# Optimization experiments

Hardware: AMD Instinct MI355X
Metric: run time of the kernel (lower is better)

Reference implementation:

```python
import jax, jax.numpy as jnp
import numpy as np
import math

B, T, E, H = 64, 256, 1024, 16
HD = E // H  # 64
EPS = 1e-5


def layernorm(x, g, b):
    mu = jnp.mean(x, axis=-1, keepdims=True)
    var = jnp.mean(jnp.square(x - mu), axis=-1, keepdims=True)
    return (x - mu) * jax.lax.rsqrt(var + EPS) * g + b


def setup_inputs() -> dict:
    key = jax.random.key(0)
    ks = jax.random.split(key, 10)
    s = 0.02
    return {
        "x": jax.random.normal(ks[0], (B, T, E), dtype=jnp.float32),
        "ln1_g": jnp.ones((E,), jnp.float32),
        "ln1_b": jnp.zeros((E,), jnp.float32),
        "wk": jax.random.normal(ks[1], (H, E, HD), jnp.float32) * s,
        "wq": jax.random.normal(ks[2], (H, E, HD), jnp.float32) * s,
        "wv": jax.random.normal(ks[3], (H, E, HD), jnp.float32) * s,
        "w_proj": jax.random.normal(ks[4], (E, E), jnp.float32) * s,
        "b_proj": jnp.zeros((E,), jnp.float32),
        "ln2_g": jnp.ones((E,), jnp.float32),
        "ln2_b": jnp.zeros((E,), jnp.float32),
        "w1": jax.random.normal(ks[5], (E, E), jnp.float32) * s,
        "b1": jnp.zeros((E,), jnp.float32),
        "w2": jax.random.normal(ks[6], (E, E), jnp.float32) * s,
        "b2": jnp.zeros((E,), jnp.float32),
    }


def reference(x, ln1_g, ln1_b, wk, wq, wv, w_proj, b_proj, ln2_g, ln2_b, w1, b1, w2, b2):
    # --- multi-head causal attention on LN1(x) ---
    h = layernorm(x, ln1_g, ln1_b)
    k = jnp.einsum('bte,hed->bhtd', h, wk)
    q = jnp.einsum('bte,hed->bhtd', h, wq)
    v = jnp.einsum('bte,hed->bhtd', h, wv)
    # NOTE: original computes k @ q^T (K.Q^T), not the standard Q.K^T -- kept faithful
    scores = jnp.einsum('bhtd,bhsd->bhts', k, q) / math.sqrt(HD)
    mask = jnp.tril(jnp.ones((T, T), dtype=bool))
    scores = jnp.where(mask, scores, -jnp.inf)
    attn_w = jax.nn.softmax(scores, axis=-1)  # dropout = identity in eval
    attn = jnp.einsum('bhts,bhsd->bhtd', attn_w, v)
    attn = attn.transpose(0, 2, 1, 3).reshape(B, T, E)  # concat heads
    x = x + attn @ w_proj + b_proj
    # --- feed-forward on LN2(x) ---
    h2 = layernorm(x, ln2_g, ln2_b)
    ff = jax.nn.relu(h2 @ w1 + b1) @ w2 + b2
    return x + ff
```

## Files before the change

kernel.cpp:

```cpp
#include <hip/hip_runtime.h>

typedef unsigned int u32;
typedef unsigned short u16;
typedef __attribute__((ext_vector_type(8))) short bf16x8;
typedef __attribute__((ext_vector_type(4))) short bf16x4;
typedef __attribute__((ext_vector_type(4))) float f32x4;

#if defined(__has_builtin)
#if __has_builtin(__builtin_amdgcn_mfma_f32_16x16x16bf16_1k)
#define HAVE_MFMA16_1K 1
#endif
#endif

#define GLOBAL_AS __attribute__((address_space(1)))
#define LDS_AS    __attribute__((address_space(3)))

#define B_   64
#define T_   256
#define E_   1024
#define H_   16
#define HD_  64
#define NTOK (B_*T_)
#define K_   1024
#define LNEPS 1e-5f

__device__ __forceinline__ u16 f2bf(float f){
  u32 x = __float_as_uint(f);
  u32 r = x + 0x7fffu + ((x >> 16) & 1u);
  return (u16)(r >> 16);
}
__device__ __forceinline__ u16 f2bf_trunc(float f){
  return (u16)(__float_as_uint(f) >> 16);
}
__device__ __forceinline__ u32 pack2(float a, float b){
  return (u32)f2bf(a) | ((u32)f2bf(b) << 16);
}

__device__ __forceinline__ void gload16(const u16* g, u16* l){
  __builtin_amdgcn_global_load_lds((const GLOBAL_AS void*)g, (LDS_AS void*)l, 16, 0, 0);
}

__global__ __launch_bounds__(256) void ln_bf16_kernel(
    const float* __restrict__ x, const float* __restrict__ g,
    const float* __restrict__ b, u16* __restrict__ o)
{
  int lane  = threadIdx.x & 63;
  int token = (blockIdx.x << 2) + (threadIdx.x >> 6);
  const float4* xr = (const float4*)(x + (size_t)token * E_);
  float4 v[4];
  float s = 0.f, ss = 0.f;
  #pragma unroll
  for (int i = 0; i < 4; ++i){
    v[i] = xr[lane + 64 * i];
    s += v[i].x + v[i].y + v[i].z + v[i].w;
    ss = fmaf(v[i].x, v[i].x, fmaf(v[i].y, v[i].y,
         fmaf(v[i].z, v[i].z, fmaf(v[i].w, v[i].w, ss))));
  }
  #pragma unroll
  for (int off = 32; off > 0; off >>= 1){
    s  += __shfl_xor(s,  off);
    ss += __shfl_xor(ss, off);
  }
  float mu   = s * (1.f / E_);
  float var  = ss * (1.f / E_) - mu * mu;
  float rstd = rsqrtf(var + LNEPS);
  const float4* gr = (const float4*)g;
  const float4* br = (const float4*)b;
  uint2* orow = (uint2*)(o + (size_t)token * E_);
  #pragma unroll
  for (int i = 0; i < 4; ++i){
    float4 gg = gr[lane + 64 * i], bb = br[lane + 64 * i];
    float y0 = (v[i].x - mu) * rstd * gg.x + bb.x;
    float y1 = (v[i].y - mu) * rstd * gg.y + bb.y;
    float y2 = (v[i].z - mu) * rstd * gg.z + bb.z;
    float y3 = (v[i].w - mu) * rstd * gg.w + bb.w;
    orow[lane + 64 * i] = make_uint2(pack2(y0, y1), pack2(y2, y3));
  }
}

__global__ __launch_bounds__(256) void convq_kernel(
    const float* __restrict__ wk, const float* __restrict__ wq,
    const float* __restrict__ wv, u16* __restrict__ o)
{
  __shared__ float tile[64 * 68];
  const int zh = blockIdx.x, z = zh >> 4, h = zh & 15;
  const int k0 = blockIdx.y << 6;
  const float* w = (z == 0 ? wk : z == 1 ? wq : wv) + (size_t)h * (E_ * HD_);
  const float qs = (z == 1) ? 0.125f : 1.0f;
  const int t = threadIdx.x;
  {
    int kr = t >> 2, d0 = (t & 3) << 4;
    const float4* src = (const float4*)(w + (size_t)(k0 + kr) * HD_ + d0);
    #pragma unroll
    for (int i = 0; i < 4; ++i)
      *(float4*)(tile + kr * 68 + d0 + 4 * i) = src[i];
  }
  __syncthreads();
  {
    const size_t nb32 = (size_t)zh * 32 + (k0 >> 5);
    #pragma unroll
    for (int u = 0; u < 2; ++u) {
      int cid = t * 2 + u;
      int dd = cid >> 3, kc = cid & 7;
      u32 wd[4];
      #pragma unroll
      for (int e2 = 0; e2 < 4; ++e2)
        wd[e2] = pack2(qs * tile[(kc * 8 + 2 * e2) * 68 + dd],
                       qs * tile[(kc * 8 + 2 * e2 + 1) * 68 + dd]);
      u16* dst = o + (nb32 + (kc >> 2)) * 2048 + (size_t)(dd >> 4) * 512
                   + (size_t)(((kc & 3) << 4) + (dd & 15)) * 8;
      *(uint4*)dst = make_uint4(wd[0], wd[1], wd[2], wd[3]);
    }
  }
}

__global__ __launch_bounds__(256) void convt3_kernel(
    const float* __restrict__ wp, const float* __restrict__ w1,
    const float* __restrict__ w2, u16* __restrict__ op,
    u16* __restrict__ o1, u16* __restrict__ o2)
{
  __shared__ float tile[64 * 68];
  const int z = blockIdx.z;
  const float* w = (z == 0 ? wp : z == 1 ? w1 : w2);
  u16* o = (z == 0 ? op : z == 1 ? o1 : o2);
  const int n0 = blockIdx.x << 6, k0 = blockIdx.y << 6;
  const int t = threadIdx.x;
  {
    int kr = t >> 2, nn = (t & 3) << 4;
    const float4* src = (const float4*)(w + (size_t)(k0 + kr) * E_ + n0 + nn);
    #pragma unroll
    for (int i = 0; i < 4; ++i)
      *(float4*)(tile + kr * 68 + nn + 4 * i) = src[i];
  }
  __syncthreads();
  {
    const size_t nb32 = (size_t)(n0 >> 6) * 32 + (k0 >> 5);
    #pragma unroll
    for (int u = 0; u < 2; ++u) {
      int cid = t * 2 + u;
      int dd = cid >> 3, kc = cid & 7;
      u32 wd[4];
      #pragma unroll
      for (int e2 = 0; e2 < 4; ++e2)
        wd[e2] = pack2(tile[(kc * 8 + 2 * e2) * 68 + dd],
                       tile[(kc * 8 + 2 * e2 + 1) * 68 + dd]);
      u16* dst = o + (nb32 + (kc >> 2)) * 2048 + (size_t)(dd >> 4) * 512
                   + (size_t)(((kc & 3) << 4) + (dd & 15)) * 8;
      *(uint4*)dst = make_uint4(wd[0], wd[1], wd[2], wd[3]);
    }
  }
}

#define MF4(I, AV, BV)                                                               \
  acc[I][0] = __builtin_amdgcn_mfma_f32_16x16x32_bf16(AV, BV[0], acc[I][0], 0, 0, 0);\
  acc[I][1] = __builtin_amdgcn_mfma_f32_16x16x32_bf16(AV, BV[1], acc[I][1], 0, 0, 0);\
  acc[I][2] = __builtin_amdgcn_mfma_f32_16x16x32_bf16(AV, BV[2], acc[I][2], 0, 0, 0);\
  acc[I][3] = __builtin_amdgcn_mfma_f32_16x16x32_bf16(AV, BV[3], acc[I][3], 0, 0, 0);

#define BLOADS(BV, SS) {                                                      \
    const u16* bp_ = Bp + (size_t)(SS) * 2048;                                \
    BV[0] = *(const bf16x8*)(bp_);                                            \
    BV[1] = *(const bf16x8*)(bp_ + 512);                                      \
    BV[2] = *(const bf16x8*)(bp_ + 1024);                                     \
    BV[3] = *(const bf16x8*)(bp_ + 1536);                                     \
  }

#define MSLICE2(SLOT, NSLOT, KA, DO_STAGE, DO_NXT, DO_BL, BS, ACUR, ATMP, ANXT, BV, BNV, VM) { \
    const u16* As_ = lds + (SLOT) * 4096;                                     \
    ATMP[0] = *(const bf16x8*)(As_ + aoffb + 1024);                           \
    ATMP[1] = *(const bf16x8*)(As_ + aoffb + 1536);                           \
    if (DO_STAGE) {                                                           \
      u16* d_ = lds + (((SLOT) + 3) & 3) * 4096;                              \
      gload16(Ag0 + (KA), d_ + tid * 8);                                      \
      gload16(Ag1 + (KA), d_ + 2048 + tid * 8);                               \
    }                                                                         \
    __builtin_amdgcn_s_setprio(1);                                            \
    MF4(0, ACUR[0], BV) MF4(1, ACUR[1], BV)                                   \
    __builtin_amdgcn_s_setprio(0);                                            \
    if (DO_NXT) {                                                             \
      const u16* An_ = lds + (NSLOT) * 4096;                                  \
      ANXT[0] = *(const bf16x8*)(An_ + aoffb);                                \
      ANXT[1] = *(const bf16x8*)(An_ + aoffb + 512);                          \
    }                                                                         \
    __builtin_amdgcn_s_setprio(1);                                            \
    MF4(2, ATMP[0], BV) MF4(3, ATMP[1], BV)                                   \
    __builtin_amdgcn_s_setprio(0);                                            \
    if (DO_BL) { BLOADS(BNV, BS) }                                            \
    VM;                                                                       \
    __builtin_amdgcn_s_barrier();                                             \
    __builtin_amdgcn_sched_barrier(0);                                        \
    asm volatile("" ::: "memory");                                            \
  }

#define VM10 asm volatile("s_waitcnt vmcnt(10)" ::: "memory")
#define VM8  asm volatile("s_waitcnt vmcnt(8)"  ::: "memory")
#define VM4  asm volatile("s_waitcnt vmcnt(4)"  ::: "memory")

template<int MODE>
__global__ __launch_bounds__(256, 3) void mgemm_kernel(
    const u16* __restrict__ A, const u16* __restrict__ Bt,
    const float* __restrict__ bias, const float* __restrict__ resid,
    float* __restrict__ Cf, u16* __restrict__ Cb, u16* __restrict__ Cb2)
{
  __shared__ __align__(16) u16 lds[16384];

  const int tid = threadIdx.x, lane = tid & 63, wid = tid >> 6;
  const int wm = wid >> 1, wn = wid & 1;
  const int l15 = lane & 15, quad = lane >> 4;

  const int b = (int)blockIdx.x;
  const int xcd = b & 7, ib = b >> 3;
  const int mloc = ib & 15, ntile = ib >> 4;
  const int row0 = (xcd * 16 + mloc) << 7;
  const int col0 = ntile << 7;

  const int sc   = (tid & 7) ^ ((tid >> 3) & 7);
  const int srow = 2 * (tid >> 3) + (sc >> 2);
  const int skof = (sc & 3) << 3;
  const u16* Ag0 = A + (size_t)(row0 + srow) * K_ + skof;
  const u16* Ag1 = Ag0 + (size_t)64 * K_;

  const int rhalf = l15 >> 1;
  const int cph   = ((((l15 & 1) << 2) | quad) ^ rhalf);
  const int aoffb = wm * 2048 + rhalf * 64 + cph * 8;

  const u16* Bp = Bt + (size_t)((col0 >> 6) + wn) * 65536 + lane * 8;

  f32x4 acc[4][4];
  #pragma unroll
  for (int i = 0; i < 4; ++i)
    #pragma unroll
    for (int j = 0; j < 4; ++j)
      acc[i][j] = (f32x4){0.f, 0.f, 0.f, 0.f};

  bf16x8 aA[2], aB[2], aT[2], bE[4], bO[4];

  #pragma unroll
  for (int t3 = 0; t3 < 3; ++t3) {
    u16* d_ = lds + t3 * 4096;
    gload16(Ag0 + t3 * 32, d_ + tid * 8);
    gload16(Ag1 + t3 * 32, d_ + 2048 + tid * 8);
  }
  BLOADS(bE, 0)
  BLOADS(bO, 1)
  asm volatile("s_waitcnt vmcnt(10)" ::: "memory");
  __builtin_amdgcn_s_barrier();
  __builtin_amdgcn_sched_barrier(0);
  asm volatile("" ::: "memory");

  aA[0] = *(const bf16x8*)(lds + aoffb);
  aA[1] = *(const bf16x8*)(lds + aoffb + 512);

  #pragma unroll 1
  for (int s = 0; s < 28; s += 2) {
    MSLICE2(s & 3, (s + 1) & 3, (s + 3) * 32, 1, 1, 1, s + 2, aA, aT, aB, bE, bE, VM10)
    MSLICE2((s + 1) & 3, (s + 2) & 3, (s + 4) * 32, 1, 1, 1, s + 3, aB, aT, aA, bO, bO, VM10)
  }
  MSLICE2(0, 1, 31 * 32, 1, 1, 1, 30, aA, aT, aB, bE, bE, VM10)
  MSLICE2(1, 2, 0,       0, 1, 1, 31, aB, aT, aA, bO, bO, VM8 )
  MSLICE2(2, 3, 0,       0, 1, 0, 0,  aA, aT, aB, bE, bE, VM4 )
  MSLICE2(3, 0, 0,       0, 0, 0, 0,  aB, aT, aA, bO, bO, (void)0)

  if (MODE == 1 || MODE == 3) {
    const int rbase = row0 + wm * 64;
    #pragma unroll
    for (int j = 0; j < 4; ++j) {
      const int n = col0 + wn * 64 + j * 16 + l15;
      const float bn = bias[n];
      #pragma unroll
      for (int i = 0; i < 4; ++i)
        #pragma unroll
        for (int r = 0; r < 4; ++r) {
          const int row = rbase + i * 16 + quad * 4 + r;
          const size_t idx = (size_t)row * E_ + n;
          float v = acc[i][j][r] + bn;
          if (MODE == 1) Cf[idx] = v + resid[idx];
          else           Cf[idx] = v + Cf[idx];
        }
    }
    return;
  }

  u16* ep = lds + wid * 4096;
  const int nb0 = col0 + wn * 64;

  if (MODE == 2) {
    #pragma unroll
    for (int j = 0; j < 4; ++j) {
      const float bn = bias[nb0 + j * 16 + l15];
      #pragma unroll
      for (int i = 0; i < 4; ++i)
        #pragma unroll
        for (int r = 0; r < 4; ++r)
          ep[(i*16 + quad*4 + r) * 64 + j*16 + l15] =
              f2bf(fmaxf(acc[i][j][r] + bn, 0.f));
    }
    const int rbase = row0 + wm * 64;
    #pragma unroll
    for (int it = 0; it < 8; ++it) {
      const int tl = it * 8 + (lane >> 3), c = lane & 7;
      uint4 v = *(const uint4*)(ep + tl * 64 + c * 8);
      *(uint4*)(Cb + (size_t)(rbase + tl) * E_ + nb0 + c * 8) = v;
    }
    return;
  }

  const int z = nb0 >> 10, hh = (nb0 >> 6) & 15;
  const int rows0 = row0 + wm * 64;
  const int bb = rows0 >> 8, tb = rows0 & 255;
  if (z < 2) {
    #pragma unroll
    for (int i = 0; i < 4; ++i)
      #pragma unroll
      for (int j = 0; j < 4; ++j)
        #pragma unroll
        for (int r = 0; r < 4; ++r)
          ep[(i*16 + quad*4 + r) * 64 + j*16 + l15] = f2bf(acc[i][j][r]);
    u16* out = (z == 0 ? Cb : Cb2) + ((size_t)(bb * H_ + hh) * T_ + tb) * HD_;
    #pragma unroll
    for (int it = 0; it < 8; ++it) {
      const int tl = it * 8 + (lane >> 3), c = lane & 7;
      uint4 v = *(const uint4*)(ep + tl * 64 + c * 8);
      *(uint4*)(out + (size_t)tl * HD_ + c * 8) = v;
    }
  } else {
    #pragma unroll
    for (int i = 0; i < 4; ++i)
      #pragma unroll
      for (int j = 0; j < 4; ++j)
        #pragma unroll
        for (int r = 0; r < 4; ++r) {
          const int tl = i*16 + quad*4 + r, d = j*16 + l15;
          const int cs = (tl >> 3) ^ (d & 7);
          ep[d * 64 + cs * 8 + (tl & 7)] = f2bf(acc[i][j][r]);
        }
    u16* out = (u16*)Cf + ((size_t)(bb * H_ + hh) * HD_) * T_;
    #pragma unroll
    for (int it = 0; it < 8; ++it) {
      const int d = it * 8 + (lane >> 3), c = lane & 7;
      const int cs = c ^ (d & 7);
      uint4 v = *(const uint4*)(ep + d * 64 + cs * 8);
      *(uint4*)(out + (size_t)d * T_ + tb + c * 8) = v;
    }
  }
}

__global__ __launch_bounds__(256, 2) void fattn_kernel(
    const u16* __restrict__ kk_, const u16* __restrict__ qq_,
    const u16* __restrict__ vt_, u16* __restrict__ out)
{
  __shared__ __align__(16) u16 Pb[4][64 * 72];
  const int tid = threadIdx.x, lane = tid & 63, wv = tid >> 6;
  const int bh = blockIdx.x * 4 + wv;
  const int tblk = 3 - (int)blockIdx.y;
  const int l15 = lane & 15, quad = lane >> 4;
  const u16* kb  = kk_ + (size_t)bh * (T_ * HD_);
  const u16* qb  = qq_ + (size_t)bh * (T_ * HD_);
  const u16* vtb = vt_ + (size_t)bh * (HD_ * T_);
  u16* Pw = Pb[wv];

  bf16x8 kf[4][2];
  #pragma unroll
  for (int i = 0; i < 4; ++i)
    #pragma unroll
    for (int c = 0; c < 2; ++c)
      kf[i][c] = *(const bf16x8*)(kb + (size_t)(tblk*64 + i*16 + l15) * HD_ + c*32 + quad*8);

  bf16x8 qf[4][2];
  #pragma unroll
  for (int j = 0; j < 4; ++j)
    #pragma unroll
    for (int c = 0; c < 2; ++c)
      qf[j][c] = *(const bf16x8*)(qb + (size_t)(j*16 + l15) * HD_ + c*32 + quad*8);

  f32x4 accT[4][4];
  float mrow[4], lrow[4];
  #pragma unroll
  for (int i = 0; i < 4; ++i) {
    #pragma unroll
    for (int jd = 0; jd < 4; ++jd) accT[jd][i] = (f32x4){0.f, 0.f, 0.f, 0.f};
    mrow[i] = -1e30f; lrow[i] = 0.f;
  }

  for (int sb = 0; sb <= tblk; ++sb) {
    f32x4 ST[4][4];
    __builtin_amdgcn_s_setprio(1);
    #pragma unroll
    for (int j = 0; j < 4; ++j)
      #pragma unroll
      for (int i = 0; i < 4; ++i) {
        f32x4 t0 = __builtin_amdgcn_mfma_f32_16x16x32_bf16(qf[j][0], kf[i][0],
                       (f32x4){0.f,0.f,0.f,0.f}, 0, 0, 0);
        ST[j][i] = __builtin_amdgcn_mfma_f32_16x16x32_bf16(qf[j][1], kf[i][1], t0, 0, 0, 0);
      }
    __builtin_amdgcn_s_setprio(0);
    if (sb < tblk) {
      #pragma unroll
      for (int j = 0; j < 4; ++j)
        #pragma unroll
        for (int c = 0; c < 2; ++c)
          qf[j][c] = *(const bf16x8*)(qb + (size_t)((sb+1)*64 + j*16 + l15) * HD_ + c*32 + quad*8);
    }
#ifdef HAVE_MFMA16_1K
    bf16x4 vv[4][4];
    #pragma unroll
    for (int j = 0; j < 4; ++j)
      #pragma unroll
      for (int jd = 0; jd < 4; ++jd)
        vv[j][jd] = *(const bf16x4*)(vtb + (size_t)(jd*16 + l15) * T_ + sb*64 + j*16 + quad*4);
#else
    bf16x8 vf[4][2];
    #pragma unroll
    for (int jd = 0; jd < 4; ++jd)
      #pragma unroll
      for (int c = 0; c < 2; ++c)
        vf[jd][c] = *(const bf16x8*)(vtb + (size_t)(jd*16 + l15) * T_ + sb*64 + c*32 + quad*8);
#endif
    if (sb == tblk) {
      #pragma unroll
      for (int j = 0; j < 4; ++j)
        #pragma unroll
        for (int i = 0; i < 4; ++i)
          #pragma unroll
          for (int r = 0; r < 4; ++r)
            if (j*16 + quad*4 + r > i*16 + l15) ST[j][i][r] = -1e30f;
    }
    #pragma unroll
    for (int i = 0; i < 4; ++i) {
      float mx = ST[0][i][0];
      #pragma unroll
      for (int j = 0; j < 4; ++j)
        #pragma unroll
        for (int r = 0; r < 4; ++r) mx = fmaxf(mx, ST[j][i][r]);
      mx = fmaxf(mx, __shfl_xor(mx, 16));
      mx = fmaxf(mx, __shfl_xor(mx, 32));
      float mn = fmaxf(mrow[i], mx);
      float al = __expf(mrow[i] - mn);
      mrow[i] = mn;
      float sm = 0.f;
      #pragma unroll
      for (int j = 0; j < 4; ++j)
        #pragma unroll
        for (int r = 0; r < 4; ++r) {
          float p = __expf(ST[j][i][r] - mn);
          ST[j][i][r] = p;
          sm += p;
        }
      sm += __shfl_xor(sm, 16);
      sm += __shfl_xor(sm, 32);
      lrow[i] = lrow[i] * al + sm;
      #pragma unroll
      for (int jd = 0; jd < 4; ++jd) accT[jd][i] = accT[jd][i] * al;
    }
#ifdef HAVE_MFMA16_1K
    #pragma unroll
    for (int j = 0; j < 4; ++j) {
      bf16x4 pfj[4];
      #pragma unroll
      for (int i = 0; i < 4; ++i)
        pfj[i] = (bf16x4){(short)f2bf_trunc(ST[j][i][0]), (short)f2bf_trunc(ST[j][i][1]),
                          (short)f2bf_trunc(ST[j][i][2]), (short)f2bf_trunc(ST[j][i][3])};
      __builtin_amdgcn_s_setprio(1);
      #pragma unroll
      for (int jd = 0; jd < 4; ++jd)
        #pragma unroll
        for (int i = 0; i < 4; ++i)
          accT[jd][i] = __builtin_amdgcn_mfma_f32_16x16x16bf16_1k(
              vv[j][jd], pfj[i], accT[jd][i], 0, 0, 0);
      __builtin_amdgcn_s_setprio(0);
    }
#else
    #pragma unroll
    for (int j = 0; j < 4; ++j)
      #pragma unroll
      for (int i = 0; i < 4; ++i)
        #pragma unroll
        for (int r = 0; r < 4; ++r)
          Pw[(i*16 + l15) * 72 + j*16 + quad*4 + r] = f2bf_trunc(ST[j][i][r]);
    bf16x8 pfB[4][2];
    #pragma unroll
    for (int i = 0; i < 4; ++i)
      #pragma unroll
      for (int c = 0; c < 2; ++c)
        pfB[i][c] = *(const bf16x8*)(Pw + (i*16 + l15) * 72 + c*32 + quad*8);
    __builtin_amdgcn_s_setprio(1);
    #pragma unroll
    for (int jd = 0; jd < 4; ++jd)
      #pragma unroll
      for (int i = 0; i < 4; ++i) {
        f32x4 t0 = __builtin_amdgcn_mfma_f32_16x16x32_bf16(vf[jd][0], pfB[i][0], accT[jd][i], 0, 0, 0);
        accT[jd][i] = __builtin_amdgcn_mfma_f32_16x16x32_bf16(vf[jd][1], pfB[i][1], t0, 0, 0, 0);
      }
    __builtin_amdgcn_s_setprio(0);
#endif
  }

  #pragma unroll
  for (int i = 0; i < 4; ++i) {
    float inv = 1.0f / lrow[i];
    #pragma unroll
    for (int jd = 0; jd < 4; ++jd)
      #pragma unroll
      for (int r = 0; r < 4; ++r)
        Pw[(i*16 + l15) * 72 + jd*16 + quad*4 + r] = f2bf(accT[jd][i][r] * inv);
  }
  {
    const int b = bh >> 4, h = bh & 15;
    const uint4* pr = (const uint4*)(Pw + lane * 72);
    uint4* og = (uint4*)(out + ((size_t)(b * T_ + tblk*64 + lane)) * E_ + h * HD_);
    #pragma unroll
    for (int k = 0; k < 8; ++k) og[k] = pr[k];
  }
}

extern "C" void kernel_launch(void* const* d_in, const int* in_sizes, int n_in,
                              void* d_out, int out_size, void* d_ws, size_t ws_size,
                              hipStream_t stream) {
  const float* x     = (const float*)d_in[0];
  const float* ln1g  = (const float*)d_in[1];
  const float* ln1b  = (const float*)d_in[2];
  const float* wk    = (const float*)d_in[3];
  const float* wq    = (const float*)d_in[4];
  const float* wv    = (const float*)d_in[5];
  const float* wproj = (const float*)d_in[6];
  const float* bproj = (const float*)d_in[7];
  const float* ln2g  = (const float*)d_in[8];
  const float* ln2b  = (const float*)d_in[9];
  const float* w1    = (const float*)d_in[10];
  const float* b1    = (const float*)d_in[11];
  const float* w2    = (const float*)d_in[12];
  const float* b2    = (const float*)d_in[13];
  float* outp = (float*)d_out;

  char* ws = (char*)d_ws;
  const size_t MB = 1024 * 1024;
  u16* wqkvT  = (u16*)(ws);
  u16* wprojT = (u16*)(ws + 6 * MB);
  u16* w1T    = (u16*)(ws + 8 * MB);
  u16* w2T    = (u16*)(ws + 10 * MB);
  u16* hb     = (u16*)(ws + 16 * MB);
  u16* kbuf   = (u16*)(ws + 48 * MB);
  u16* qbuf   = (u16*)(ws + 80 * MB);
  u16* vtbuf  = (u16*)d_out;

  convq_kernel<<<dim3(48, 16), 256, 0, stream>>>(wk, wq, wv, wqkvT);
  convt3_kernel<<<dim3(16, 16, 3), 256, 0, stream>>>(wproj, w1, w2, wprojT, w1T, w2T);

  ln_bf16_kernel<<<NTOK/4, 256, 0, stream>>>(x, ln1g, ln1b, hb);
  mgemm_kernel<0><<<3072, 256, 0, stream>>>(
      hb, wqkvT, nullptr, nullptr, (float*)vtbuf, kbuf, qbuf);
  fattn_kernel<<<dim3(B_*H_/4, 4), 256, 0, stream>>>(kbuf, qbuf, vtbuf, hb);
  mgemm_kernel<1><<<1024, 256, 0, stream>>>(
      hb, wprojT, bproj, x, outp, nullptr, nullptr);
  ln_bf16_kernel<<<NTOK/4, 256, 0, stream>>>(outp, ln2g, ln2b, kbuf);
  mgemm_kernel<2><<<1024, 256, 0, stream>>>(
      kbuf, w1T, b1, nullptr, nullptr, qbuf, nullptr);
  mgemm_kernel<3><<<1024, 256, 0, stream>>>(
      qbuf, w2T, b2, nullptr, outp, nullptr, nullptr);
}
```

Measured before the change: 478.5 us.

## Enlarge GEMM tiles to 256x256 with 8 waves and double-buffered K=64 stages

```diff
diff --git a/kernel.cpp b/kernel.cpp
--- a/kernel.cpp
+++ b/kernel.cpp
@@ -157,6 +157,12 @@
   acc[I][2] = __builtin_amdgcn_mfma_f32_16x16x32_bf16(AV, BV[2], acc[I][2], 0, 0, 0);\
   acc[I][3] = __builtin_amdgcn_mfma_f32_16x16x32_bf16(AV, BV[3], acc[I][3], 0, 0, 0);
 
+#define MC(IB, AV, BV)                                                        \
+    __builtin_amdgcn_s_setprio(1);                                            \
+    MF4((IB)+0, AV[0], BV) MF4((IB)+1, AV[1], BV)                             \
+    MF4((IB)+2, AV[2], BV) MF4((IB)+3, AV[3], BV)                             \
+    __builtin_amdgcn_s_setprio(0);
+
 #define BLOADS(BV, SS) {                                                      \
     const u16* bp_ = Bp + (size_t)(SS) * 2048;                                \
     BV[0] = *(const bf16x8*)(bp_);                                            \
@@ -165,110 +171,104 @@
     BV[3] = *(const bf16x8*)(bp_ + 1536);                                     \
   }
 
-#define MSLICE2(SLOT, NSLOT, KA, DO_STAGE, DO_NXT, DO_BL, BS, ACUR, ATMP, ANXT, BV, BNV, VM) { \
-    const u16* As_ = lds + (SLOT) * 4096;                                     \
-    ATMP[0] = *(const bf16x8*)(As_ + aoffb + 1024);                           \
-    ATMP[1] = *(const bf16x8*)(As_ + aoffb + 1536);                           \
-    if (DO_STAGE) {                                                           \
-      u16* d_ = lds + (((SLOT) + 3) & 3) * 4096;                              \
-      gload16(Ag0 + (KA), d_ + tid * 8);                                      \
-      gload16(Ag1 + (KA), d_ + 2048 + tid * 8);                               \
-    }                                                                         \
-    __builtin_amdgcn_s_setprio(1);                                            \
-    MF4(0, ACUR[0], BV) MF4(1, ACUR[1], BV)                                   \
-    __builtin_amdgcn_s_setprio(0);                                            \
-    if (DO_NXT) {                                                             \
-      const u16* An_ = lds + (NSLOT) * 4096;                                  \
-      ANXT[0] = *(const bf16x8*)(An_ + aoffb);                                \
-      ANXT[1] = *(const bf16x8*)(An_ + aoffb + 512);                          \
-    }                                                                         \
-    __builtin_amdgcn_s_setprio(1);                                            \
-    MF4(2, ATMP[0], BV) MF4(3, ATMP[1], BV)                                   \
-    __builtin_amdgcn_s_setprio(0);                                            \
-    if (DO_BL) { BLOADS(BNV, BS) }                                            \
-    VM;                                                                       \
+#define ARD4(DST, AB, IB, S)                                                  \
+    DST[0] = *(const bf16x8*)((AB) + ((IB)+0)*1024 + prl*128 + (S)*8);        \
+    DST[1] = *(const bf16x8*)((AB) + ((IB)+1)*1024 + prl*128 + ((S)^8)*8);    \
+    DST[2] = *(const bf16x8*)((AB) + ((IB)+2)*1024 + prl*128 + (S)*8);        \
+    DST[3] = *(const bf16x8*)((AB) + ((IB)+3)*1024 + prl*128 + ((S)^8)*8);
+
+#define GTILE(T, DOS) {                                                       \
+    const int d_ = (T) & 1;                                                   \
+    const u16* Ab = lds + d_*16384 + wm*8192;                                 \
+    u16* sd = lds + (d_^1)*16384;                                             \
+    ARD4(aX, Ab, 0, s00v)                                                     \
+    if (DOS) { gload16(Ag00 + ((T)+1)*64, sd + tid*8);                        \
+               gload16(Ag01 + ((T)+1)*64, sd + 4096 + tid*8); }               \
+    ARD4(aY, Ab, 4, s00v)                                                     \
+    if (DOS) { gload16(Ag10 + ((T)+1)*64, sd + 8192 + tid*8);                 \
+               gload16(Ag11 + ((T)+1)*64, sd + 12288 + tid*8);                \
+               __builtin_amdgcn_sched_barrier(0x38F); }                       \
+    MC(0, aX, bE)                                                             \
+    ARD4(aX, Ab, 0, s01v)                                                     \
+    MC(4, aY, bE)                                                             \
+    if (DOS) { BLOADS(bE, 2*(T)+2) }                                          \
+    ARD4(aY, Ab, 4, s01v)                                                     \
+    MC(0, aX, bO)                                                             \
+    MC(4, aY, bO)                                                             \
+    if (DOS) { BLOADS(bO, 2*(T)+3)                                            \
+               asm volatile("s_waitcnt vmcnt(8)" ::: "memory"); }             \
     __builtin_amdgcn_s_barrier();                                             \
     __builtin_amdgcn_sched_barrier(0);                                        \
     asm volatile("" ::: "memory");                                            \
   }
 
-#define VM10 asm volatile("s_waitcnt vmcnt(10)" ::: "memory")
-#define VM8  asm volatile("s_waitcnt vmcnt(8)"  ::: "memory")
-#define VM4  asm volatile("s_waitcnt vmcnt(4)"  ::: "memory")
-
 template<int MODE>
-__global__ __launch_bounds__(256, 3) void mgemm_kernel(
+__global__ __launch_bounds__(512, 2) void mgemm_kernel(
     const u16* __restrict__ A, const u16* __restrict__ Bt,
     const float* __restrict__ bias, const float* __restrict__ resid,
     float* __restrict__ Cf, u16* __restrict__ Cb, u16* __restrict__ Cb2)
 {
-  __shared__ __align__(16) u16 lds[16384];
+  __shared__ __align__(16) u16 lds[32768];
 
   const int tid = threadIdx.x, lane = tid & 63, wid = tid >> 6;
-  const int wm = wid >> 1, wn = wid & 1;
+  const int wm = wid >> 2, wn = wid & 3;
   const int l15 = lane & 15, quad = lane >> 4;
 
   const int b = (int)blockIdx.x;
   const int xcd = b & 7, ib = b >> 3;
-  const int mloc = ib & 15, ntile = ib >> 4;
-  const int row0 = (xcd * 16 + mloc) << 7;
-  const int col0 = ntile << 7;
-
-  const int sc   = (tid & 7) ^ ((tid >> 3) & 7);
-  const int srow = 2 * (tid >> 3) + (sc >> 2);
-  const int skof = (sc & 3) << 3;
-  const u16* Ag0 = A + (size_t)(row0 + srow) * K_ + skof;
-  const u16* Ag1 = Ag0 + (size_t)64 * K_;
-
-  const int rhalf = l15 >> 1;
-  const int cph   = ((((l15 & 1) << 2) | quad) ^ rhalf);
-  const int aoffb = wm * 2048 + rhalf * 64 + cph * 8;
+  const int mloc = ib & 7, ntile = ib >> 3;
+  const int row0 = (xcd * 8 + mloc) << 8;
+  const int col0 = ntile << 8;
+
+  const int cid1 = 512 + tid;
+  const int pr0 = tid >> 4,  sp0 = (tid & 15)  ^ (pr0 & 15);
+  const int pr1 = cid1 >> 4, sp1 = (cid1 & 15) ^ (pr1 & 15);
+  const int r0 = 2*pr0 + (sp0 >> 3), c0 = sp0 & 7;
+  const int r1 = 2*pr1 + (sp1 >> 3), c1 = sp1 & 7;
+  const u16* Ag00 = A + (size_t)(row0 + r0) * K_ + c0 * 8;
+  const u16* Ag01 = A + (size_t)(row0 + r1) * K_ + c1 * 8;
+  const u16* Ag10 = Ag00 + (size_t)128 * K_;
+  const u16* Ag11 = Ag01 + (size_t)128 * K_;
+
+  const int prl  = l15 >> 1;
+  const int s00v = (((l15 & 1) << 3) + quad) ^ prl;
+  const int s01v = (((l15 & 1) << 3) + 4 + quad) ^ prl;
 
   const u16* Bp = Bt + (size_t)((col0 >> 6) + wn) * 65536 + lane * 8;
 
-  f32x4 acc[4][4];
-  #pragma unroll
-  for (int i = 0; i < 4; ++i)
+  f32x4 acc[8][4];
+  #pragma unroll
+  for (int i = 0; i < 8; ++i)
     #pragma unroll
     for (int j = 0; j < 4; ++j)
       acc[i][j] = (f32x4){0.f, 0.f, 0.f, 0.f};
 
-  bf16x8 aA[2], aB[2], aT[2], bE[4], bO[4];
-
-  #pragma unroll
-  for (int t3 = 0; t3 < 3; ++t3) {
-    u16* d_ = lds + t3 * 4096;
-    gload16(Ag0 + t3 * 32, d_ + tid * 8);
-    gload16(Ag1 + t3 * 32, d_ + 2048 + tid * 8);
-  }
+  bf16x8 aX[4], aY[4], bE[4], bO[4];
+
+  gload16(Ag00, lds + tid * 8);
+  gload16(Ag01, lds + 4096 + tid * 8);
+  gload16(Ag10, lds + 8192 + tid * 8);
+  gload16(Ag11, lds + 12288 + tid * 8);
+  __builtin_amdgcn_sched_barrier(0x38F);
   BLOADS(bE, 0)
   BLOADS(bO, 1)
-  asm volatile("s_waitcnt vmcnt(10)" ::: "memory");
+  asm volatile("s_waitcnt vmcnt(8)" ::: "memory");
   __builtin_amdgcn_s_barrier();
   __builtin_amdgcn_sched_barrier(0);
   asm volatile("" ::: "memory");
 
-  aA[0] = *(const bf16x8*)(lds + aoffb);
-  aA[1] = *(const bf16x8*)(lds + aoffb + 512);
-
   #pragma unroll 1
-  for (int s = 0; s < 28; s += 2) {
-    MSLICE2(s & 3, (s + 1) & 3, (s + 3) * 32, 1, 1, 1, s + 2, aA, aT, aB, bE, bE, VM10)
-    MSLICE2((s + 1) & 3, (s + 2) & 3, (s + 4) * 32, 1, 1, 1, s + 3, aB, aT, aA, bO, bO, VM10)
-  }
-  MSLICE2(0, 1, 31 * 32, 1, 1, 1, 30, aA, aT, aB, bE, bE, VM10)
-  MSLICE2(1, 2, 0,       0, 1, 1, 31, aB, aT, aA, bO, bO, VM8 )
-  MSLICE2(2, 3, 0,       0, 1, 0, 0,  aA, aT, aB, bE, bE, VM4 )
-  MSLICE2(3, 0, 0,       0, 0, 0, 0,  aB, aT, aA, bO, bO, (void)0)
+  for (int t = 0; t < 15; ++t) GTILE(t, 1)
+  GTILE(15, 0)
 
   if (MODE == 1 || MODE == 3) {
-    const int rbase = row0 + wm * 64;
+    const int rbase = row0 + wm * 128;
     #pragma unroll
     for (int j = 0; j < 4; ++j) {
       const int n = col0 + wn * 64 + j * 16 + l15;
       const float bn = bias[n];
       #pragma unroll
-      for (int i = 0; i < 4; ++i)
+      for (int i = 0; i < 8; ++i)
         #pragma unroll
         for (int r = 0; r < 4; ++r) {
           const int row = rbase + i * 16 + quad * 4 + r;
@@ -285,62 +285,71 @@
   const int nb0 = col0 + wn * 64;
 
   if (MODE == 2) {
-    #pragma unroll
-    for (int j = 0; j < 4; ++j) {
-      const float bn = bias[nb0 + j * 16 + l15];
-      #pragma unroll
-      for (int i = 0; i < 4; ++i)
-        #pragma unroll
-        for (int r = 0; r < 4; ++r)
-          ep[(i*16 + quad*4 + r) * 64 + j*16 + l15] =
-              f2bf(fmaxf(acc[i][j][r] + bn, 0.f));
-    }
-    const int rbase = row0 + wm * 64;
-    #pragma unroll
-    for (int it = 0; it < 8; ++it) {
-      const int tl = it * 8 + (lane >> 3), c = lane & 7;
-      uint4 v = *(const uint4*)(ep + tl * 64 + c * 8);
-      *(uint4*)(Cb + (size_t)(rbase + tl) * E_ + nb0 + c * 8) = v;
+    const int rbase = row0 + wm * 128;
+    #pragma unroll
+    for (int p = 0; p < 2; ++p) {
+      #pragma unroll
+      for (int j = 0; j < 4; ++j) {
+        const float bn = bias[nb0 + j * 16 + l15];
+        #pragma unroll
+        for (int il = 0; il < 4; ++il)
+          #pragma unroll
+          for (int r = 0; r < 4; ++r)
+            ep[(il*16 + quad*4 + r) * 64 + j*16 + l15] =
+                f2bf(fmaxf(acc[p*4 + il][j][r] + bn, 0.f));
+      }
+      #pragma unroll
+      for (int it = 0; it < 8; ++it) {
+        const int tl = it * 8 + (lane >> 3), c = lane & 7;
+        uint4 v = *(const uint4*)(ep + tl * 64 + c * 8);
+        *(uint4*)(Cb + (size_t)(rbase + p*64 + tl) * E_ + nb0 + c * 8) = v;
+      }
     }
     return;
   }
 
   const int z = nb0 >> 10, hh = (nb0 >> 6) & 15;
-  const int rows0 = row0 + wm * 64;
+  const int rows0 = row0 + wm * 128;
   const int bb = rows0 >> 8, tb = rows0 & 255;
   if (z < 2) {
-    #pragma unroll
-    for (int i = 0; i < 4; ++i)
-      #pragma unroll
-      for (int j = 0; j < 4; ++j)
-        #pragma unroll
-        for (int r = 0; r < 4; ++r)
-          ep[(i*16 + quad*4 + r) * 64 + j*16 + l15] = f2bf(acc[i][j][r]);
     u16* out = (z == 0 ? Cb : Cb2) + ((size_t)(bb * H_ + hh) * T_ + tb) * HD_;
     #pragma unroll
-    for (int it = 0; it < 8; ++it) {
-      const int tl = it * 8 + (lane >> 3), c = lane & 7;
-      uint4 v = *(const uint4*)(ep + tl * 64 + c * 8);
-      *(uint4*)(out + (size_t)tl * HD_ + c * 8) = v;
+    for (int p = 0; p < 2; ++p) {
+      #pragma unroll
+      for (int il = 0; il < 4; ++il)
+        #pragma unroll
+        for (int j = 0; j < 4; ++j)
+          #pragma unroll
+          for (int r = 0; r < 4; ++r)
+            ep[(il*16 + quad*4 + r) * 64 + j*16 + l15] = f2bf(acc[p*4 + il][j][r]);
+      #pragma unroll
+      for (int it = 0; it < 8; ++it) {
+        const int tl = it * 8 + (lane >> 3), c = lane & 7;
+        uint4 v = *(const uint4*)(ep + tl * 64 + c * 8);
+        *(uint4*)(out + (size_t)(p*64 + tl) * HD_ + c * 8) = v;
+      }
     }
   } else {
-    #pragma unroll
-    for (int i = 0; i < 4; ++i)
-      #pragma unroll
-      for (int j = 0; j < 4; ++j)
-        #pragma unroll
-        for (int r = 0; r < 4; ++r) {
-          const int tl = i*16 + quad*4 + r, d = j*16 + l15;
-          const int cs = (tl >> 3) ^ (d & 7);
-          ep[d * 64 + cs * 8 + (tl & 7)] = f2bf(acc[i][j][r]);
-        }
     u16* out = (u16*)Cf + ((size_t)(bb * H_ + hh) * HD_) * T_;
     #pragma unroll
-    for (int it = 0; it < 8; ++it) {
-      const int d = it * 8 + (lane >> 3), c = lane & 7;
-      const int cs = c ^ (d & 7);
-      uint4 v = *(const uint4*)(ep + d * 64 + cs * 8);
-      *(uint4*)(out + (size_t)d * T_ + tb + c * 8) = v;
+    for (int p = 0; p < 2; ++p) {
+      #pragma unroll
+      for (int il = 0; il < 4; ++il)
+        #pragma unroll
+        for (int j = 0; j < 4; ++j)
+          #pragma unroll
+          for (int r = 0; r < 4; ++r) {
+            const int tl = il*16 + quad*4 + r, dd = j*16 + l15;
+            const int cs = (tl >> 3) ^ (dd & 7);
+            ep[dd * 64 + cs * 8 + (tl & 7)] = f2bf(acc[p*4 + il][j][r]);
+          }
+      #pragma unroll
+      for (int it = 0; it < 8; ++it) {
+        const int dd = it * 8 + (lane >> 3), c = lane & 7;
+        const int cs = c ^ (dd & 7);
+        uint4 v = *(const uint4*)(ep + dd * 64 + cs * 8);
+        *(uint4*)(out + (size_t)dd * T_ + tb + p*64 + c * 8) = v;
+      }
     }
   }
 }
@@ -547,14 +556,14 @@
   convt3_kernel<<<dim3(16, 16, 3), 256, 0, stream>>>(wproj, w1, w2, wprojT, w1T, w2T);
 
   ln_bf16_kernel<<<NTOK/4, 256, 0, stream>>>(x, ln1g, ln1b, hb);
-  mgemm_kernel<0><<<3072, 256, 0, stream>>>(
+  mgemm_kernel<0><<<768, 512, 0, stream>>>(
       hb, wqkvT, nullptr, nullptr, (float*)vtbuf, kbuf, qbuf);
   fattn_kernel<<<dim3(B_*H_/4, 4), 256, 0, stream>>>(kbuf, qbuf, vtbuf, hb);
-  mgemm_kernel<1><<<1024, 256, 0, stream>>>(
+  mgemm_kernel<1><<<256, 512, 0, stream>>>(
       hb, wprojT, bproj, x, outp, nullptr, nullptr);
   ln_bf16_kernel<<<NTOK/4, 256, 0, stream>>>(outp, ln2g, ln2b, kbuf);
-  mgemm_kernel<2><<<1024, 256, 0, stream>>>(
+  mgemm_kernel<2><<<256, 512, 0, stream>>>(
       kbuf, w1T, b1, nullptr, nullptr, qbuf, nullptr);
-  mgemm_kernel<3><<<1024, 256, 0, stream>>>(
+  mgemm_kernel<3><<<256, 512, 0, stream>>>(
       qbuf, w2T, b2, nullptr, outp, nullptr, nullptr);
 }
```

After: 468.4 us. -2.1%, faster.
